# Kernel optimization log

Hardware: AMD Instinct MI355X
Metric: run time of the kernel (lower is better)

Reference implementation:

```python
import jax, jax.numpy as jnp
import numpy as np

N_LVL = 127.0   # 8-bit symmetric: 2**(8-1) - 1
BN_EPS = 1e-5
PATCH = 16


def quant_act(x):
    """Per-tensor 8-bit symmetric quant-dequant (HAWQ-style QuantAct, dynamic range)."""
    scale = jnp.max(jnp.abs(x)) / N_LVL
    xq = jnp.clip(jnp.round(x / scale), -N_LVL, N_LVL) * scale
    return xq, scale


def setup_inputs() -> dict:
    key = jax.random.key(0)
    k0, k1, k2, k3, k4 = jax.random.split(key, 5)
    B, C, H = 128, 3, 224
    dim = 768
    x = jax.random.normal(k0, (B, C, H, H), jnp.float32)
    W = jax.random.normal(k1, (dim, C, PATCH, PATCH), jnp.float32) * 0.02
    b = jax.random.normal(k2, (dim,), jnp.float32) * 0.02
    gamma = jnp.ones((dim,), jnp.float32)
    beta = jnp.zeros((dim,), jnp.float32)
    run_mean = jax.random.normal(k3, (dim,), jnp.float32) * 0.1
    run_var = jax.random.uniform(k4, (dim,), jnp.float32, 0.5, 1.5)
    return {"x": x, "W": W, "b": b, "gamma": gamma, "beta": beta,
            "run_mean": run_mean, "run_var": run_var}


def reference(x, W, b, gamma, beta, run_mean, run_var):
    # --- quant_input ---
    x_q, pre_s = quant_act(x)                                   # [B,3,224,224], scalar
    # --- QuantConv2d: per-out-channel 8-bit symmetric weight quant ---
    w_scale = jnp.max(jnp.abs(W), axis=(1, 2, 3), keepdims=True) / N_LVL  # [dim,1,1,1]
    w_int = jnp.round(W / w_scale)
    x_int = x_q / pre_s                                         # integer-valued activations
    comb_s = w_scale[:, 0, 0, 0] * pre_s                        # [dim] conv output scale
    b_int = jnp.round(b / comb_s)
    y = jax.lax.conv_general_dilated(
        x_int, w_int, window_strides=(PATCH, PATCH), padding='VALID',
        dimension_numbers=('NCHW', 'OIHW', 'NCHW'))             # [B,768,14,14]
    y = (y + b_int[None, :, None, None]) * comb_s[None, :, None, None]
    # --- quant_act_conv ---
    y, _ = quant_act(y)
    # --- GELU (torch nn.GELU default: exact erf) ---
    y = jax.nn.gelu(y, approximate=False)
    # --- qact1 ---
    y, _ = quant_act(y)
    # --- BatchNorm2d (eval mode, running stats) ---
    inv = gamma / jnp.sqrt(run_var + BN_EPS)
    y = y * inv[None, :, None, None] + (beta - run_mean * inv)[None, :, None, None]
    # --- qact2 ---
    y, act_scale = quant_act(y)
    return y, act_scale
```

## Files before the change

### kernel.cpp

```cpp
#include <hip/hip_runtime.h>

#define TOT   19267584
#define MROWS 25088
#define KD    768
#define NPB   196
#define CHW   150528

typedef unsigned int uint;
typedef __attribute__((ext_vector_type(4))) int i32x4;

#define OFF_AQ   0ull
#define OFF_WQ   19267584ull
#define OFF_WSC  19857408ull
#define OFF_INV  19860480ull
#define OFF_SHF  19863552ull
#define OFF_PA   19866624ull
#define OFF_PB   19871328ull
#define OFF_CMN  19876032ull
#define OFF_CMX  19879104ull
#define OFF_SC   19882176ull

__device__ __forceinline__ float wave_max(float v) {
#pragma unroll
  for (int off = 32; off > 0; off >>= 1) v = fmaxf(v, __shfl_xor(v, off));
  return v;
}

__device__ __forceinline__ float block_max(float v) {
  __shared__ float red[4];
  v = wave_max(v);
  if ((threadIdx.x & 63) == 0) red[threadIdx.x >> 6] = v;
  __syncthreads();
  return fmaxf(fmaxf(red[0], red[1]), fmaxf(red[2], red[3]));
}

__global__ void k_maxabs(const float* __restrict__ x, float* __restrict__ pA) {
  const int i0 = blockIdx.x * 256 + threadIdx.x;
  const float4* x4 = (const float4*)x;
  float m = 0.f;
#pragma unroll
  for (int j = 0; j < 16; j += 4) {
    float4 a = x4[i0 + (j + 0) * 301056];
    float4 b = x4[i0 + (j + 1) * 301056];
    float4 c = x4[i0 + (j + 2) * 301056];
    float4 d = x4[i0 + (j + 3) * 301056];
    m = fmaxf(m, fmaxf(fmaxf(fabsf(a.x), fabsf(a.y)), fmaxf(fabsf(a.z), fabsf(a.w))));
    m = fmaxf(m, fmaxf(fmaxf(fabsf(b.x), fabsf(b.y)), fmaxf(fabsf(b.z), fabsf(b.w))));
    m = fmaxf(m, fmaxf(fmaxf(fabsf(c.x), fabsf(c.y)), fmaxf(fabsf(c.z), fabsf(c.w))));
    m = fmaxf(m, fmaxf(fmaxf(fabsf(d.x), fabsf(d.y)), fmaxf(fabsf(d.z), fabsf(d.w))));
  }
  float bm = block_max(m);
  if (threadIdx.x == 0) pA[blockIdx.x] = bm;
}

__global__ void k_combine(const float* __restrict__ p, int n, uint* __restrict__ dst) {
  float m = 0.f;
  for (int i = threadIdx.x; i < n; i += 256) m = fmaxf(m, p[i]);
  float bm = block_max(m);
  if (threadIdx.x == 0) *dst = __float_as_uint(bm);
}

__global__ void k_wquant(const float* __restrict__ W, const float* __restrict__ gamma,
                         const float* __restrict__ beta, const float* __restrict__ rmean,
                         const float* __restrict__ rvar, signed char* __restrict__ wq,
                         float* __restrict__ wscale, float* __restrict__ inv_,
                         float* __restrict__ shf) {
  const int oc = blockIdx.x;
  const float* row = W + oc * KD;
  float m = 0.f;
  for (int k = threadIdx.x; k < KD; k += 256) m = fmaxf(m, fabsf(row[k]));
  const float ws_ = block_max(m) / 127.0f;
  for (int k = threadIdx.x; k < KD; k += 256)
    wq[oc * KD + k] = (signed char)(int)rintf(row[k] / ws_);
  if (threadIdx.x == 0) {
    wscale[oc] = ws_;
    float iv = gamma[oc] / sqrtf(rvar[oc] + 1e-5f);
    inv_[oc] = iv;
    shf[oc] = __fsub_rn(beta[oc], __fmul_rn(rmean[oc], iv));
  }
}

__global__ void k_im2col(const float* __restrict__ x, const uint* __restrict__ sc,
                         signed char* __restrict__ aq) {
  const float ps = __uint_as_float(sc[0]) / 127.0f;
  const int u = blockIdx.x * 256 + threadIdx.x;
  const int p = u / 48, r = u - p * 48;
  const int c = r >> 4, kh = r & 15;
  const int b = p / NPB, pp = p - b * NPB;
  const int ph = pp / 14, pw = pp - ph * 14;
  const float* src = x + (((b * 3 + c) * 224 + ph * 16 + kh) * 224 + pw * 16);
  float4 v0 = *(const float4*)(src);
  float4 v1 = *(const float4*)(src + 4);
  float4 v2 = *(const float4*)(src + 8);
  float4 v3 = *(const float4*)(src + 12);
#define Q8(v) ((int)fminf(fmaxf(rintf((v) / ps), -127.f), 127.f) & 255)
  uint4 o;
  o.x = Q8(v0.x) | (Q8(v0.y) << 8) | (Q8(v0.z) << 16) | ((uint)Q8(v0.w) << 24);
  o.y = Q8(v1.x) | (Q8(v1.y) << 8) | (Q8(v1.z) << 16) | ((uint)Q8(v1.w) << 24);
  o.z = Q8(v2.x) | (Q8(v2.y) << 8) | (Q8(v2.z) << 16) | ((uint)Q8(v2.w) << 24);
  o.w = Q8(v3.x) | (Q8(v3.y) << 8) | (Q8(v3.z) << 16) | ((uint)Q8(v3.w) << 24);
#undef Q8
  *(uint4*)(aq + (size_t)p * KD + (r << 4)) = o;
}

__device__ __forceinline__ void gl_lds16(const void* g, void* l) {
  __builtin_amdgcn_global_load_lds((const __attribute__((address_space(1))) void*)g,
                                   (__attribute__((address_space(3))) void*)l, 16, 0, 0);
}

__global__ __launch_bounds__(256) void k_gemm(const signed char* __restrict__ aq,
                                              const signed char* __restrict__ wq,
                                              const float* __restrict__ bias,
                                              const float* __restrict__ wscale,
                                              const uint* __restrict__ sc,
                                              float* __restrict__ y,
                                              float* __restrict__ pB) {
  __shared__ __align__(16) signed char lA[2][8192];
  __shared__ __align__(16) signed char lB[2][8192];
  const int tid = threadIdx.x, lane = tid & 63, wv = tid >> 6;
  const int bsw = (blockIdx.x & 7) * 147 + (blockIdx.x >> 3);
  const int bm = bsw / 6, bn = bsw - 6 * (bsw / 6);
  const int wr = wv >> 1, wc = wv & 1;
  const float ps = __uint_as_float(sc[0]) / 127.0f;

  const int ci0 = wv * 2, ci1 = wv * 2 + 1;
  const int rr0 = ci0 * 16 + (lane >> 2);
  const int rr1 = ci1 * 16 + (lane >> 2);
  const int bo = (((lane & 3) ^ ((lane >> 2) & 3)) << 4);
  const signed char* gA0 = aq + (size_t)(bm * 128 + rr0) * KD + bo;
  const signed char* gA1 = aq + (size_t)(bm * 128 + rr1) * KD + bo;
  const signed char* gB0 = wq + (size_t)(bn * 128 + rr0) * KD + bo;
  const signed char* gB1 = wq + (size_t)(bn * 128 + rr1) * KD + bo;

  i32x4 acc[4][4];
#pragma unroll
  for (int m = 0; m < 4; ++m)
#pragma unroll
    for (int n = 0; n < 4; ++n) acc[m][n] = (i32x4){0, 0, 0, 0};

  const int rbase = lane & 15;
  const int kg = (((lane >> 4) << 4)) ^ ((lane & 3) << 4);

  gl_lds16(gA0, &lA[0][ci0 * 1024]);
  gl_lds16(gA1, &lA[0][ci1 * 1024]);
  gl_lds16(gB0, &lB[0][ci0 * 1024]);
  gl_lds16(gB1, &lB[0][ci1 * 1024]);
  __syncthreads();

  int cur = 0;
  for (int t = 0; t < 12; ++t) {
    if (t < 11) {
      const int kk = (t + 1) * 64;
      gl_lds16(gA0 + kk, &lA[cur ^ 1][ci0 * 1024]);
      gl_lds16(gA1 + kk, &lA[cur ^ 1][ci1 * 1024]);
      gl_lds16(gB0 + kk, &lB[cur ^ 1][ci0 * 1024]);
      gl_lds16(gB1 + kk, &lB[cur ^ 1][ci1 * 1024]);
    }
    i32x4 af[4], bfr[4];
#pragma unroll
    for (int m = 0; m < 4; ++m)
      af[m] = *(const i32x4*)&lA[cur][(wr * 64 + m * 16 + rbase) * 64 + kg];
#pragma unroll
    for (int n = 0; n < 4; ++n)
      bfr[n] = *(const i32x4*)&lB[cur][(wc * 64 + n * 16 + rbase) * 64 + kg];
#pragma unroll
    for (int m = 0; m < 4; ++m)
#pragma unroll
      for (int n = 0; n < 4; ++n)
        acc[m][n] = __builtin_amdgcn_mfma_i32_16x16x64_i8(af[m], bfr[n], acc[m][n], 0, 0, 0);
    __syncthreads();
    cur ^= 1;
  }

  float lmax = 0.f;
  const int prow = (lane >> 4) << 2;
#pragma unroll
  for (int n = 0; n < 4; ++n) {
    const int oc = bn * 128 + wc * 64 + n * 16 + rbase;
    const float comb = wscale[oc] * ps;
    const float bint = rintf(bias[oc] / comb);
#pragma unroll
    for (int m = 0; m < 4; ++m) {
      const int p0 = bm * 128 + wr * 64 + m * 16 + prow;
      const int img = p0 / 196;
      const int q = p0 - img * 196;
      float4 o;
      o.x = ((float)acc[m][n][0] + bint) * comb;
      o.y = ((float)acc[m][n][1] + bint) * comb;
      o.z = ((float)acc[m][n][2] + bint) * comb;
      o.w = ((float)acc[m][n][3] + bint) * comb;
      lmax = fmaxf(lmax, fmaxf(fmaxf(fabsf(o.x), fabsf(o.y)), fmaxf(fabsf(o.z), fabsf(o.w))));
      *(float4*)(y + (size_t)img * CHW + (size_t)oc * 196 + q) = o;
    }
  }
  float bm_ = block_max(lmax);
  if (tid == 0) pB[blockIdx.x] = bm_;
}

__global__ void k_gelu_chan(const float* __restrict__ y, const uint* __restrict__ sc,
                            signed char* __restrict__ k1, float* __restrict__ chmn,
                            float* __restrict__ chmx) {
  const int c = blockIdx.x;
  const float s1 = __uint_as_float(sc[1]) / 127.0f;
  __shared__ float tab[255];
  for (int t = threadIdx.x; t < 255; t += 256) {
    float y1 = (float)(t - 127) * s1;
    float e = erff(y1 * 0.70710678118654752f);
    tab[t] = (y1 * (e + 1.0f)) * 0.5f;
  }
  __syncthreads();
  float mn = 1e30f, mx = -1e30f;
  const float4* y4 = (const float4*)y;
  char4* k4 = (char4*)k1;
#define ADDR(u) ((size_t)((u) / 49) * (CHW / 4) + (size_t)c * 49 + ((u) - ((u) / 49) * 49))
#define PROC(v, a4)                                                        \
  {                                                                        \
    int ia = (int)fminf(fmaxf(rintf((v).x / s1), -127.f), 127.f);          \
    int ib = (int)fminf(fmaxf(rintf((v).y / s1), -127.f), 127.f);          \
    int ic = (int)fminf(fmaxf(rintf((v).z / s1), -127.f), 127.f);          \
    int id = (int)fminf(fmaxf(rintf((v).w / s1), -127.f), 127.f);          \
    char4 kk;                                                              \
    kk.x = (signed char)ia; kk.y = (signed char)ib;                        \
    kk.z = (signed char)ic; kk.w = (signed char)id;                        \
    k4[a4] = kk;                                                           \
    float ga = tab[ia + 127], gb = tab[ib + 127];                          \
    float gc = tab[ic + 127], gd = tab[id + 127];                          \
    mn = fminf(mn, fminf(fminf(ga, gb), fminf(gc, gd)));                   \
    mx = fmaxf(mx, fmaxf(fmaxf(ga, gb), fmaxf(gc, gd)));                   \
  }
  for (int r = 0; r < 6; ++r) {
    const int u0 = threadIdx.x + r * 1024;
    const size_t a0 = ADDR(u0), a1 = ADDR(u0 + 256), a2 = ADDR(u0 + 512), a3 = ADDR(u0 + 768);
    float4 v0 = y4[a0];
    float4 v1 = y4[a1];
    float4 v2 = y4[a2];
    float4 v3 = y4[a3];
    PROC(v0, a0) PROC(v1, a1) PROC(v2, a2) PROC(v3, a3)
  }
  if (threadIdx.x < 128) {
    const int u = 6144 + threadIdx.x;
    const size_t a = ADDR(u);
    float4 v = y4[a];
    PROC(v, a)
  }
#undef PROC
#undef ADDR
  __shared__ float rmn[4], rmx[4];
#pragma unroll
  for (int off = 32; off > 0; off >>= 1) {
    mn = fminf(mn, __shfl_xor(mn, off));
    mx = fmaxf(mx, __shfl_xor(mx, off));
  }
  const int lane = threadIdx.x & 63, wvx = threadIdx.x >> 6;
  if (lane == 0) { rmn[wvx] = mn; rmx[wvx] = mx; }
  __syncthreads();
  if (threadIdx.x == 0) {
    chmn[c] = fminf(fminf(rmn[0], rmn[1]), fminf(rmn[2], rmn[3]));
    chmx[c] = fmaxf(fmaxf(rmx[0], rmx[1]), fmaxf(rmx[2], rmx[3]));
  }
}

__global__ void k_scales(const float* __restrict__ chmn, const float* __restrict__ chmx,
                         const float* __restrict__ inv_, const float* __restrict__ shf,
                         uint* __restrict__ sc) {
  __shared__ float sred[4];
  __shared__ float s2sh;
  const int tid = threadIdx.x;
  float m2 = 0.f;
  for (int c = tid; c < 768; c += 256)
    m2 = fmaxf(m2, fmaxf(fabsf(chmn[c]), fabsf(chmx[c])));
  m2 = wave_max(m2);
  if ((tid & 63) == 0) sred[tid >> 6] = m2;
  __syncthreads();
  if (tid == 0) {
    float s2 = fmaxf(fmaxf(sred[0], sred[1]), fmaxf(sred[2], sred[3])) / 127.0f;
    s2sh = s2;
    sc[2] = __float_as_uint(s2);
  }
  __syncthreads();
  const float s2 = s2sh;
  float m4 = 0.f;
  for (int c = tid; c < 768; c += 256) {
    float iv = inv_[c], sh = shf[c];
    float a = fminf(fmaxf(rintf(chmn[c] / s2), -127.f), 127.f) * s2;
    float b = fminf(fmaxf(rintf(chmx[c] / s2), -127.f), 127.f) * s2;
    float ya = __fadd_rn(__fmul_rn(a, iv), sh);
    float yb = __fadd_rn(__fmul_rn(b, iv), sh);
    m4 = fmaxf(m4, fmaxf(fabsf(ya), fabsf(yb)));
  }
  m4 = wave_max(m4);
  __syncthreads();
  if ((tid & 63) == 0) sred[tid >> 6] = m4;
  __syncthreads();
  if (tid == 0)
    sc[3] = __float_as_uint(fmaxf(fmaxf(sred[0], sred[1]), fmaxf(sred[2], sred[3])) / 127.0f);
}

__global__ void k_final(const signed char* __restrict__ k1, const uint* __restrict__ sc,
                        const float* __restrict__ inv_, const float* __restrict__ shf,
                        float* __restrict__ out) {
  __shared__ float tab[255];
  const float s1 = __uint_as_float(sc[1]) / 127.0f;
  const float s2 = __uint_as_float(sc[2]);
  const float s3 = __uint_as_float(sc[3]);
  for (int t = threadIdx.x; t < 255; t += 256) {
    float y1 = (float)(t - 127) * s1;
    float e = erff(y1 * 0.70710678118654752f);
    float y2 = (y1 * (e + 1.0f)) * 0.5f;
    float q2 = fminf(fmaxf(rintf(y2 / s2), -127.f), 127.f);
    tab[t] = q2 * s2;
  }
  __syncthreads();
  const int i = blockIdx.x * 256 + threadIdx.x;
  const char4* k4 = (const char4*)k1;
  char4 a0 = k4[i];
  char4 a1 = k4[i + 1204224];
  char4 a2 = k4[i + 2 * 1204224];
  char4 a3 = k4[i + 3 * 1204224];
  float4* out4 = (float4*)out;
#define FIN(kk, idx)                                                       \
  {                                                                        \
    int c = ((idx) / 49) % 768;                                            \
    float iv = inv_[c], sh = shf[c];                                       \
    float fa = __fadd_rn(__fmul_rn(tab[kk.x + 127], iv), sh);              \
    float fb = __fadd_rn(__fmul_rn(tab[kk.y + 127], iv), sh);              \
    float fc = __fadd_rn(__fmul_rn(tab[kk.z + 127], iv), sh);              \
    float fd = __fadd_rn(__fmul_rn(tab[kk.w + 127], iv), sh);              \
    float4 o;                                                              \
    o.x = fminf(fmaxf(rintf(fa / s3), -127.f), 127.f) * s3;                \
    o.y = fminf(fmaxf(rintf(fb / s3), -127.f), 127.f) * s3;                \
    o.z = fminf(fmaxf(rintf(fc / s3), -127.f), 127.f) * s3;                \
    o.w = fminf(fmaxf(rintf(fd / s3), -127.f), 127.f) * s3;                \
    out4[idx] = o;                                                         \
  }
  FIN(a0, i)
  FIN(a1, i + 1204224)
  FIN(a2, i + 2 * 1204224)
  FIN(a3, i + 3 * 1204224)
#undef FIN
  if (blockIdx.x == 0 && threadIdx.x == 0) out[TOT] = s3;
}

extern "C" void kernel_launch(void* const* d_in, const int* in_sizes, int n_in,
                              void* d_out, int out_size, void* d_ws, size_t ws_size,
                              hipStream_t stream) {
  const float* x     = (const float*)d_in[0];
  const float* W     = (const float*)d_in[1];
  const float* bias  = (const float*)d_in[2];
  const float* gamma = (const float*)d_in[3];
  const float* beta  = (const float*)d_in[4];
  const float* rmean = (const float*)d_in[5];
  const float* rvar  = (const float*)d_in[6];
  float* out = (float*)d_out;
  char* ws = (char*)d_ws;

  signed char* aq  = (signed char*)(ws + OFF_AQ);
  signed char* wq  = (signed char*)(ws + OFF_WQ);
  float* wsc  = (float*)(ws + OFF_WSC);
  float* inv_ = (float*)(ws + OFF_INV);
  float* shf  = (float*)(ws + OFF_SHF);
  float* pA   = (float*)(ws + OFF_PA);
  float* pB   = (float*)(ws + OFF_PB);
  float* cmn  = (float*)(ws + OFF_CMN);
  float* cmx  = (float*)(ws + OFF_CMX);
  uint*  sc   = (uint*)(ws + OFF_SC);
  signed char* k1 = (signed char*)(ws + OFF_AQ);

  k_maxabs<<<1176, 256, 0, stream>>>(x, pA);
  k_wquant<<<768, 256, 0, stream>>>(W, gamma, beta, rmean, rvar, wq, wsc, inv_, shf);
  k_combine<<<1, 256, 0, stream>>>(pA, 1176, sc + 0);
  k_im2col<<<4704, 256, 0, stream>>>(x, sc, aq);
  k_gemm<<<1176, 256, 0, stream>>>(aq, wq, bias, wsc, sc, out, pB);
  k_combine<<<1, 256, 0, stream>>>(pB, 1176, sc + 1);
  k_gelu_chan<<<768, 256, 0, stream>>>(out, sc, k1, cmn, cmx);
  k_scales<<<1, 256, 0, stream>>>(cmn, cmx, inv_, shf, sc);
  k_final<<<4704, 256, 0, stream>>>(k1, sc, inv_, shf, out);
}
```

Baseline: 124.8 us.

## Fold scalar reductions into consumers and triple-buffer GEMM LDS pipeline

Removes the three single-block reduction kernels (two combine passes and k_scales). Each consumer kernel now redundantly reduces the partial-max arrays itself, which cuts launch overhead and serial one-block stages. The int8 GEMM moves from a double- to a triple-buffered global-to-LDS pipeline with explicit vmcnt waits and raw barriers, and changes the LDS swizzle pattern. The cost is extra redundant reads of the partials in every block and more LDS per block, which may reduce occupancy.

```diff
diff --git a/kernel.cpp b/kernel.cpp
--- a/kernel.cpp
+++ b/kernel.cpp
@@ -18,7 +18,6 @@
 #define OFF_PB   19871328ull
 #define OFF_CMN  19876032ull
 #define OFF_CMX  19879104ull
-#define OFF_SC   19882176ull
 
 __device__ __forceinline__ float wave_max(float v) {
 #pragma unroll
@@ -29,6 +28,7 @@
 __device__ __forceinline__ float block_max(float v) {
   __shared__ float red[4];
   v = wave_max(v);
+  __syncthreads();
   if ((threadIdx.x & 63) == 0) red[threadIdx.x >> 6] = v;
   __syncthreads();
   return fmaxf(fmaxf(red[0], red[1]), fmaxf(red[2], red[3]));
@@ -51,13 +51,6 @@
   }
   float bm = block_max(m);
   if (threadIdx.x == 0) pA[blockIdx.x] = bm;
-}
-
-__global__ void k_combine(const float* __restrict__ p, int n, uint* __restrict__ dst) {
-  float m = 0.f;
-  for (int i = threadIdx.x; i < n; i += 256) m = fmaxf(m, p[i]);
-  float bm = block_max(m);
-  if (threadIdx.x == 0) *dst = __float_as_uint(bm);
 }
 
 __global__ void k_wquant(const float* __restrict__ W, const float* __restrict__ gamma,
@@ -80,9 +73,11 @@
   }
 }
 
-__global__ void k_im2col(const float* __restrict__ x, const uint* __restrict__ sc,
+__global__ void k_im2col(const float* __restrict__ x, const float* __restrict__ pA,
                          signed char* __restrict__ aq) {
-  const float ps = __uint_as_float(sc[0]) / 127.0f;
+  float mm = 0.f;
+  for (int i = threadIdx.x; i < 1176; i += 256) mm = fmaxf(mm, pA[i]);
+  const float ps = block_max(mm) / 127.0f;
   const int u = blockIdx.x * 256 + threadIdx.x;
   const int p = u / 48, r = u - p * 48;
   const int c = r >> 4, kh = r & 15;
@@ -112,21 +107,20 @@
                                               const signed char* __restrict__ wq,
                                               const float* __restrict__ bias,
                                               const float* __restrict__ wscale,
-                                              const uint* __restrict__ sc,
+                                              const float* __restrict__ pA,
                                               float* __restrict__ y,
                                               float* __restrict__ pB) {
-  __shared__ __align__(16) signed char lA[2][8192];
-  __shared__ __align__(16) signed char lB[2][8192];
+  __shared__ __align__(16) signed char lA[3][8192];
+  __shared__ __align__(16) signed char lB[3][8192];
   const int tid = threadIdx.x, lane = tid & 63, wv = tid >> 6;
   const int bsw = (blockIdx.x & 7) * 147 + (blockIdx.x >> 3);
   const int bm = bsw / 6, bn = bsw - 6 * (bsw / 6);
   const int wr = wv >> 1, wc = wv & 1;
-  const float ps = __uint_as_float(sc[0]) / 127.0f;
 
   const int ci0 = wv * 2, ci1 = wv * 2 + 1;
   const int rr0 = ci0 * 16 + (lane >> 2);
   const int rr1 = ci1 * 16 + (lane >> 2);
-  const int bo = (((lane & 3) ^ ((lane >> 2) & 3)) << 4);
+  const int bo = (((lane & 3) ^ ((lane >> 3) & 3)) << 4);
   const signed char* gA0 = aq + (size_t)(bm * 128 + rr0) * KD + bo;
   const signed char* gA1 = aq + (size_t)(bm * 128 + rr1) * KD + bo;
   const signed char* gB0 = wq + (size_t)(bn * 128 + rr0) * KD + bo;
@@ -139,38 +133,45 @@
     for (int n = 0; n < 4; ++n) acc[m][n] = (i32x4){0, 0, 0, 0};
 
   const int rbase = lane & 15;
-  const int kg = (((lane >> 4) << 4)) ^ ((lane & 3) << 4);
-
-  gl_lds16(gA0, &lA[0][ci0 * 1024]);
-  gl_lds16(gA1, &lA[0][ci1 * 1024]);
-  gl_lds16(gB0, &lB[0][ci0 * 1024]);
-  gl_lds16(gB1, &lB[0][ci1 * 1024]);
-  __syncthreads();
-
-  int cur = 0;
+  const int kg = (((lane >> 4) << 4)) ^ (((lane >> 1) & 3) << 4);
+
+#define STAGE(T, B)                                   \
+  {                                                   \
+    const int kk_ = (T) * 64;                         \
+    gl_lds16(gA0 + kk_, &lA[B][ci0 * 1024]);          \
+    gl_lds16(gA1 + kk_, &lA[B][ci1 * 1024]);          \
+    gl_lds16(gB0 + kk_, &lB[B][ci0 * 1024]);          \
+    gl_lds16(gB1 + kk_, &lB[B][ci1 * 1024]);          \
+  }
+
+  STAGE(0, 0)
+  STAGE(1, 1)
+#pragma unroll
   for (int t = 0; t < 12; ++t) {
-    if (t < 11) {
-      const int kk = (t + 1) * 64;
-      gl_lds16(gA0 + kk, &lA[cur ^ 1][ci0 * 1024]);
-      gl_lds16(gA1 + kk, &lA[cur ^ 1][ci1 * 1024]);
-      gl_lds16(gB0 + kk, &lB[cur ^ 1][ci0 * 1024]);
-      gl_lds16(gB1 + kk, &lB[cur ^ 1][ci1 * 1024]);
-    }
+    if (t < 11) { asm volatile("s_waitcnt vmcnt(4)" ::: "memory"); }
+    else        { asm volatile("s_waitcnt vmcnt(0)" ::: "memory"); }
+    __builtin_amdgcn_s_barrier();
+    __builtin_amdgcn_sched_barrier(0);
+    const int b = t % 3;
     i32x4 af[4], bfr[4];
 #pragma unroll
     for (int m = 0; m < 4; ++m)
-      af[m] = *(const i32x4*)&lA[cur][(wr * 64 + m * 16 + rbase) * 64 + kg];
+      af[m] = *(const i32x4*)&lA[b][(wr * 64 + m * 16 + rbase) * 64 + kg];
 #pragma unroll
     for (int n = 0; n < 4; ++n)
-      bfr[n] = *(const i32x4*)&lB[cur][(wc * 64 + n * 16 + rbase) * 64 + kg];
+      bfr[n] = *(const i32x4*)&lB[b][(wc * 64 + n * 16 + rbase) * 64 + kg];
+    if (t < 10) STAGE(t + 2, (t + 2) % 3)
 #pragma unroll
     for (int m = 0; m < 4; ++m)
 #pragma unroll
       for (int n = 0; n < 4; ++n)
         acc[m][n] = __builtin_amdgcn_mfma_i32_16x16x64_i8(af[m], bfr[n], acc[m][n], 0, 0, 0);
-    __syncthreads();
-    cur ^= 1;
-  }
+  }
+#undef STAGE
+
+  float mm = 0.f;
+  for (int i = tid; i < 1176; i += 256) mm = fmaxf(mm, pA[i]);
+  const float ps = block_max(mm) / 127.0f;
 
   float lmax = 0.f;
   const int prow = (lane >> 4) << 2;
@@ -197,11 +198,13 @@
   if (tid == 0) pB[blockIdx.x] = bm_;
 }
 
-__global__ void k_gelu_chan(const float* __restrict__ y, const uint* __restrict__ sc,
+__global__ void k_gelu_chan(const float* __restrict__ y, const float* __restrict__ pB,
                             signed char* __restrict__ k1, float* __restrict__ chmn,
                             float* __restrict__ chmx) {
   const int c = blockIdx.x;
-  const float s1 = __uint_as_float(sc[1]) / 127.0f;
+  float mm = 0.f;
+  for (int i = threadIdx.x; i < 1176; i += 256) mm = fmaxf(mm, pB[i]);
+  const float s1 = block_max(mm) / 127.0f;
   __shared__ float tab[255];
   for (int t = threadIdx.x; t < 255; t += 256) {
     float y1 = (float)(t - 127) * s1;
@@ -260,27 +263,19 @@
   }
 }
 
-__global__ void k_scales(const float* __restrict__ chmn, const float* __restrict__ chmx,
-                         const float* __restrict__ inv_, const float* __restrict__ shf,
-                         uint* __restrict__ sc) {
-  __shared__ float sred[4];
-  __shared__ float s2sh;
-  const int tid = threadIdx.x;
+__global__ void k_final(const signed char* __restrict__ k1, const float* __restrict__ pB,
+                        const float* __restrict__ chmn, const float* __restrict__ chmx,
+                        const float* __restrict__ inv_, const float* __restrict__ shf,
+                        float* __restrict__ out) {
+  float mm = 0.f;
+  for (int i = threadIdx.x; i < 1176; i += 256) mm = fmaxf(mm, pB[i]);
+  const float s1 = block_max(mm) / 127.0f;
   float m2 = 0.f;
-  for (int c = tid; c < 768; c += 256)
+  for (int c = threadIdx.x; c < 768; c += 256)
     m2 = fmaxf(m2, fmaxf(fabsf(chmn[c]), fabsf(chmx[c])));
-  m2 = wave_max(m2);
-  if ((tid & 63) == 0) sred[tid >> 6] = m2;
-  __syncthreads();
-  if (tid == 0) {
-    float s2 = fmaxf(fmaxf(sred[0], sred[1]), fmaxf(sred[2], sred[3])) / 127.0f;
-    s2sh = s2;
-    sc[2] = __float_as_uint(s2);
-  }
-  __syncthreads();
-  const float s2 = s2sh;
+  const float s2 = block_max(m2) / 127.0f;
   float m4 = 0.f;
-  for (int c = tid; c < 768; c += 256) {
+  for (int c = threadIdx.x; c < 768; c += 256) {
     float iv = inv_[c], sh = shf[c];
     float a = fminf(fmaxf(rintf(chmn[c] / s2), -127.f), 127.f) * s2;
     float b = fminf(fmaxf(rintf(chmx[c] / s2), -127.f), 127.f) * s2;
@@ -288,21 +283,9 @@
     float yb = __fadd_rn(__fmul_rn(b, iv), sh);
     m4 = fmaxf(m4, fmaxf(fabsf(ya), fabsf(yb)));
   }
-  m4 = wave_max(m4);
-  __syncthreads();
-  if ((tid & 63) == 0) sred[tid >> 6] = m4;
-  __syncthreads();
-  if (tid == 0)
-    sc[3] = __float_as_uint(fmaxf(fmaxf(sred[0], sred[1]), fmaxf(sred[2], sred[3])) / 127.0f);
-}
-
-__global__ void k_final(const signed char* __restrict__ k1, const uint* __restrict__ sc,
-                        const float* __restrict__ inv_, const float* __restrict__ shf,
-                        float* __restrict__ out) {
+  const float s3 = block_max(m4) / 127.0f;
+
   __shared__ float tab[255];
-  const float s1 = __uint_as_float(sc[1]) / 127.0f;
-  const float s2 = __uint_as_float(sc[2]);
-  const float s3 = __uint_as_float(sc[3]);
   for (int t = threadIdx.x; t < 255; t += 256) {
     float y1 = (float)(t - 127) * s1;
     float e = erff(y1 * 0.70710678118654752f);
@@ -363,16 +346,12 @@
   float* pB   = (float*)(ws + OFF_PB);
   float* cmn  = (float*)(ws + OFF_CMN);
   float* cmx  = (float*)(ws + OFF_CMX);
-  uint*  sc   = (uint*)(ws + OFF_SC);
   signed char* k1 = (signed char*)(ws + OFF_AQ);
 
   k_maxabs<<<1176, 256, 0, stream>>>(x, pA);
   k_wquant<<<768, 256, 0, stream>>>(W, gamma, beta, rmean, rvar, wq, wsc, inv_, shf);
-  k_combine<<<1, 256, 0, stream>>>(pA, 1176, sc + 0);
-  k_im2col<<<4704, 256, 0, stream>>>(x, sc, aq);
-  k_gemm<<<1176, 256, 0, stream>>>(aq, wq, bias, wsc, sc, out, pB);
-  k_combine<<<1, 256, 0, stream>>>(pB, 1176, sc + 1);
-  k_gelu_chan<<<768, 256, 0, stream>>>(out, sc, k1, cmn, cmx);
-  k_scales<<<1, 256, 0, stream>>>(cmn, cmx, inv_, shf, sc);
-  k_final<<<4704, 256, 0, stream>>>(k1, sc, inv_, shf, out);
-}
+  k_im2col<<<4704, 256, 0, stream>>>(x, pA, aq);
+  k_gemm<<<1176, 256, 0, stream>>>(aq, wq, bias, wsc, pA, out, pB);
+  k_gelu_chan<<<768, 256, 0, stream>>>(out, pB, k1, cmn, cmx);
+  k_final<<<4704, 256, 0, stream>>>(k1, pB, cmn, cmx, inv_, shf, out);
+}
```

Result: no change. 125.6 us (+0.7%).
